# Kernel tuning notes

Measured on AMD Instinct MI355X. Metric: run time of the kernel, lower is better.

The kernel has to match this reference:

```python
import jax, jax.numpy as jnp
import numpy as np
from jax import lax

EPS = 1e-5
HEADS = 8

def chan_ln(x, g):
    # ChanLayerNorm: normalize over channel dim (1), biased variance, gamma only
    mean = jnp.mean(x, axis=1, keepdims=True)
    var = jnp.var(x, axis=1, keepdims=True)
    return (x - mean) * lax.rsqrt(var + EPS) * g[None, :, None, None]

def conv1x1(x, w):  # w: [O, C]
    return jnp.einsum('bchw,oc->bohw', x, w)

def dwconv3(x, w):  # depthwise 3x3, w: [C,1,3,3]
    return lax.conv_general_dilated(x, w, (1, 1), 'SAME',
                                    dimension_numbers=('NCHW', 'OIHW', 'NCHW'),
                                    feature_group_count=x.shape[1])


def setup_inputs() -> dict:
    key = jax.random.key(0)
    ks = jax.random.split(key, 8)
    B, DIM, H, W = 8, 512, 96, 96
    INNER = 256
    s = 0.02
    return {
        'fmap': jax.random.normal(ks[0], (B, DIM, H, W), jnp.float32),
        'norm_g': jnp.ones((DIM,), jnp.float32),
        'q_w1': jax.random.normal(ks[1], (INNER, DIM), jnp.float32) * s,
        'q_wd': jax.random.normal(ks[2], (INNER, 1, 3, 3), jnp.float32) * s,
        'k_w1': jax.random.normal(ks[3], (INNER, DIM), jnp.float32) * s,
        'k_wd': jax.random.normal(ks[4], (INNER, 1, 3, 3), jnp.float32) * s,
        'v_w1': jax.random.normal(ks[5], (INNER, DIM), jnp.float32) * s,
        'v_wd': jax.random.normal(ks[6], (INNER, 1, 3, 3), jnp.float32) * s,
        'out_w': jax.random.normal(ks[7], (DIM, INNER), jnp.float32) * s,
        'out_norm_g': jnp.ones((DIM,), jnp.float32),
    }


def reference(fmap, norm_g, q_w1, q_wd, k_w1, k_wd, v_w1, v_wd, out_w, out_norm_g):
    B, C, H, W = fmap.shape
    inner = q_w1.shape[0]
    dh = inner // HEADS
    scale = dh ** -0.5

    x = chan_ln(fmap, norm_g)
    # dropout is identity in eval mode
    q = dwconv3(conv1x1(x, q_w1), q_wd)
    k = dwconv3(conv1x1(x, k_w1), k_wd)
    v = dwconv3(conv1x1(x, v_w1), v_wd)

    def split(t):  # [B, h*c, H, W] -> [B*h, N, c]
        return t.reshape(B, HEADS, dh, H * W).transpose(0, 1, 3, 2).reshape(B * HEADS, H * W, dh)

    q, k, v = split(q), split(k), split(v)
    q = jax.nn.softmax(q, axis=-1) * scale   # softmax over feature dim
    k = jax.nn.softmax(k, axis=-2)           # softmax over spatial dim

    context = jnp.einsum('bnd,bne->bde', k, v)   # [B*h, d, d]
    out = jnp.einsum('bnd,bde->bne', q, context) # [B*h, N, d]

    out = out.reshape(B, HEADS, H * W, dh).transpose(0, 1, 3, 2).reshape(B, inner, H, W)
    out = jax.nn.silu(out)
    out = conv1x1(out, out_w)
    return chan_ln(out, out_norm_g)
```

## Files before the change

kernel.cpp:

```cpp
#include <hip/hip_runtime.h>
#include <math.h>

#define BATCH 8
#define GB 4
#define CDIM 512
#define HGT 96
#define WID 96
#define HWN (HGT*WID)
#define INNER 256
#define NHEADS 8
#define DH 32
#define NPIX (BATCH*HWN)
#define EPSLN 1e-5f
#define QSCALE 0.17677669529663687f
#define PATHSZ ((size_t)GB*INNER*HWN)

typedef __bf16 bf16_t;
typedef bf16_t bf16x8 __attribute__((ext_vector_type(8)));
typedef float  f32x4  __attribute__((ext_vector_type(4)));

__device__ __forceinline__ void load_lds16(const bf16_t* gp, bf16_t* lp) {
    __builtin_amdgcn_global_load_lds(
        (const __attribute__((address_space(1))) unsigned int*)gp,
        (__attribute__((address_space(3))) unsigned int*)lp,
        16, 0, 0);
}

__global__ __launch_bounds__(256) void wsum_kernel(const float* __restrict__ qw,
                                                   const float* __restrict__ kw,
                                                   const float* __restrict__ vw,
                                                   const float* __restrict__ g,
                                                   float* __restrict__ wsum) {
    int i = blockIdx.x * 256 + threadIdx.x;
    if (i >= 3 * INNER) return;
    const float* w = (i < INNER) ? qw : (i < 2 * INNER) ? kw : vw;
    int o = i % INNER;
    float s = 0.f;
    for (int c = 0; c < CDIM; ++c) s += w[o * CDIM + c] * g[c];
    wsum[i] = s;
}

__global__ __launch_bounds__(256) void wprep_kernel(const float* __restrict__ qw,
                                                    const float* __restrict__ kw,
                                                    const float* __restrict__ vw,
                                                    const float* __restrict__ g,
                                                    const float* __restrict__ ow,
                                                    bf16_t* __restrict__ WB,
                                                    bf16_t* __restrict__ OWB) {
    int i = blockIdx.x * 256 + threadIdx.x;
    const int PS = INNER * CDIM;
    if (i < 3 * PS) {
        int m = i / PS;
        int idx = i % PS;
        int c = idx % CDIM;
        const float* w = (m == 0) ? qw : (m == 1) ? kw : vw;
        float val = w[idx] * g[c];
        bf16_t h = (bf16_t)val;
        bf16_t l = (bf16_t)(val - (float)h);
        WB[(size_t)(2 * m) * PS + idx] = h;
        WB[(size_t)(2 * m + 1) * PS + idx] = l;
    } else {
        int idx = i - 3 * PS;
        float val = ow[idx];
        bf16_t h = (bf16_t)val;
        bf16_t l = (bf16_t)(val - (float)h);
        OWB[idx] = h;
        OWB[PS + idx] = l;
    }
}

__global__ __launch_bounds__(256) void transpose_split_kernel(const float* __restrict__ X,
                                                              bf16_t* __restrict__ Fh,
                                                              bf16_t* __restrict__ Fl,
                                                              float* __restrict__ S1,
                                                              float* __restrict__ S2,
                                                              int pbase) {
    __shared__ float T[64][65];
    __shared__ float Ps[4][64], Ps2[4][64];
    int bb = blockIdx.z;
    int n0 = blockIdx.x * 64;
    int c0 = blockIdx.y * 64;
    const float* Xb = X + ((size_t)bb * CDIM) * HWN;
    int tid = threadIdx.x;
    {
        int nl4 = (tid & 15) * 4;
        int cl = tid >> 4;
        #pragma unroll
        for (int it = 0; it < 4; ++it) {
            int cc = cl + 16 * it;
            f32x4 v = *(const f32x4*)&Xb[(size_t)(c0 + cc) * HWN + n0 + nl4];
            T[cc][nl4]     = v.x;
            T[cc][nl4 + 1] = v.y;
            T[cc][nl4 + 2] = v.z;
            T[cc][nl4 + 3] = v.w;
        }
    }
    int tx = tid & 63, ty = tid >> 6;
    __syncthreads();
    {
        float s = 0.f, s2 = 0.f;
        #pragma unroll
        for (int c = ty * 16; c < ty * 16 + 16; ++c) {
            float v = T[c][tx];
            s += v; s2 += v * v;
        }
        Ps[ty][tx] = s; Ps2[ty][tx] = s2;
    }
    __syncthreads();
    if (tid < 64) {
        float a = Ps[0][tid] + Ps[1][tid] + Ps[2][tid] + Ps[3][tid];
        float b = Ps2[0][tid] + Ps2[1][tid] + Ps2[2][tid] + Ps2[3][tid];
        int p = pbase + bb * HWN + n0 + tid;
        atomicAdd(&S1[p], a);
        atomicAdd(&S2[p], b);
    }
    int nr = tid >> 3;
    int c8 = (tid & 7) << 3;
    size_t obase = ((size_t)bb * HWN) * CDIM;
    #pragma unroll
    for (int half = 0; half < 2; ++half) {
        int n = nr + 32 * half;
        bf16x8 hv, lv;
        #pragma unroll
        for (int j = 0; j < 8; ++j) {
            float v = T[c8 + j][n];
            bf16_t h = (bf16_t)v;
            hv[j] = h;
            lv[j] = (bf16_t)(v - (float)h);
        }
        size_t off = obase + (size_t)(n0 + n) * CDIM + c0 + c8;
        *(bf16x8*)&Fh[off] = hv;
        *(bf16x8*)&Fl[off] = lv;
    }
}

template <int KDIM, int MROWS, int MODE>
__global__ __launch_bounds__(256) void mfma_gemm_kernel(const bf16_t* __restrict__ Wbase,
                                                        const bf16_t* __restrict__ Bh,
                                                        const bf16_t* __restrict__ Bl,
                                                        float* __restrict__ S1,
                                                        float* __restrict__ S2,
                                                        const float* __restrict__ wsum,
                                                        int pbase,
                                                        float* __restrict__ Ybase) {
    __shared__ bf16_t sA[2][128 * 32];
    __shared__ bf16_t sB[2][128 * 32];
    int bb = blockIdx.z;
    int n0 = blockIdx.x * 128;
    const int PS = INNER * CDIM;
    int o0, path;
    const bf16_t *Ah, *Al;
    float* Y;
    if (MODE == 0) {
        path = blockIdx.y >> 1;
        o0 = (blockIdx.y & 1) * 128;
        Ah = Wbase + (size_t)(2 * path) * PS;
        Al = Wbase + (size_t)(2 * path + 1) * PS;
        Y = Ybase + (size_t)path * PATHSZ;
        wsum += path * INNER;
    } else {
        path = 0;
        o0 = blockIdx.y * 128;
        Ah = Wbase;
        Al = Wbase + PS;
        Y = Ybase;
    }
    int tid = threadIdx.x;
    int wv = tid >> 6, ln = tid & 63;
    int wm = wv >> 1, wn = wv & 1;
    int quad = ln >> 4, lm = ln & 15;
    int srow = ln >> 2;
    int scol = ((ln & 3) ^ ((ln >> 3) & 3)) * 8;
    int qs = (quad ^ ((lm >> 1) & 3)) * 8;

    const bf16_t* Bhb = Bh + ((size_t)bb * HWN) * KDIM;
    const bf16_t* Blb = Bl + ((size_t)bb * HWN) * KDIM;

    f32x4 acc[4][4] = {};

    for (int c0 = 0; c0 < KDIM; c0 += 32) {
        __syncthreads();
        #pragma unroll
        for (int t = 0; t < 2; ++t) {
            int inst = wv * 2 + t;
            int row = inst * 16 + srow;
            size_t goA = (size_t)(o0 + row) * KDIM + c0 + scol;
            size_t goB = (size_t)(n0 + row) * KDIM + c0 + scol;
            load_lds16(&Ah[goA],  &sA[0][inst * 512]);
            load_lds16(&Al[goA],  &sA[1][inst * 512]);
            load_lds16(&Bhb[goB], &sB[0][inst * 512]);
            load_lds16(&Blb[goB], &sB[1][inst * 512]);
        }
        __syncthreads();

        bf16x8 afh[4], afl[4], bfh[4], bfl[4];
        #pragma unroll
        for (int i = 0; i < 4; ++i) {
            int o_l = wm * 64 + i * 16 + lm;
            afh[i] = *(const bf16x8*)&sA[0][o_l * 32 + qs];
            afl[i] = *(const bf16x8*)&sA[1][o_l * 32 + qs];
            int n_l = wn * 64 + i * 16 + lm;
            bfh[i] = *(const bf16x8*)&sB[0][n_l * 32 + qs];
            bfl[i] = *(const bf16x8*)&sB[1][n_l * 32 + qs];
        }
        #pragma unroll
        for (int i = 0; i < 4; ++i)
            #pragma unroll
            for (int j = 0; j < 4; ++j) {
                acc[i][j] = __builtin_amdgcn_mfma_f32_16x16x32_bf16(afh[i], bfh[j], acc[i][j], 0, 0, 0);
                acc[i][j] = __builtin_amdgcn_mfma_f32_16x16x32_bf16(afh[i], bfl[j], acc[i][j], 0, 0, 0);
                acc[i][j] = __builtin_amdgcn_mfma_f32_16x16x32_bf16(afl[i], bfh[j], acc[i][j], 0, 0, 0);
            }
    }

    float* Yb = Y + ((size_t)bb * MROWS) * HWN;
    __shared__ float Sn[128], Sn2[128];
    if (MODE == 1) {
        if (tid < 128) Sn[tid] = 0.f; else Sn2[tid - 128] = 0.f;
        __syncthreads();
    }
    #pragma unroll
    for (int j = 0; j < 4; ++j) {
        int nl = wn * 64 + j * 16 + lm;
        int n = n0 + nl;
        float mn = 0.f, rs = 0.f;
        if (MODE == 0) {
            int p = pbase + bb * HWN + n;
            float s1 = S1[p], s2 = S2[p];
            mn = s1 * (1.0f / CDIM);
            float var = s2 * (1.0f / CDIM) - mn * mn;
            rs = rsqrtf(var + EPSLN);
        }
        float js = 0.f, js2 = 0.f;
        #pragma unroll
        for (int i = 0; i < 4; ++i) {
            #pragma unroll
            for (int r = 0; r < 4; ++r) {
                int o = o0 + wm * 64 + i * 16 + quad * 4 + r;
                float v = acc[i][j][r];
                if (MODE == 0) v = rs * (v - mn * wsum[o]);
                Yb[(size_t)o * HWN + n] = v;
                if (MODE == 1) { js += v; js2 += v * v; }
            }
        }
        if (MODE == 1) {
            atomicAdd(&Sn[nl], js);
            atomicAdd(&Sn2[nl], js2);
        }
    }
    if (MODE == 1) {
        __syncthreads();
        if (tid < 128) {
            int p = pbase + bb * HWN + n0 + tid;
            atomicAdd(&S1[p], Sn[tid]);
            atomicAdd(&S2[p], Sn2[tid]);
        }
    }
}

__global__ __launch_bounds__(192) void dwconv_kernel(const float* __restrict__ A3,
                                                     const float* __restrict__ qwd,
                                                     const float* __restrict__ kwd,
                                                     const float* __restrict__ vwd,
                                                     float* __restrict__ D3,
                                                     float* __restrict__ Ssum,
                                                     int bo) {
    int c = blockIdx.y;
    int zz = blockIdx.z;
    int path = zz >> 2;
    int bb = zz & 3;
    const float* wf = ((path == 0) ? qwd : (path == 1) ? kwd : vwd) + c * 9;
    float w[9];
    #pragma unroll
    for (int j = 0; j < 9; ++j) w[j] = wf[j];

    int x0 = threadIdx.x * 4;
    int y0 = (blockIdx.x * 8 + threadIdx.y) * 2;
    bool hasL = (x0 != 0);
    bool hasR = (x0 != WID - 4);

    const float* bp = A3 + (size_t)path * PATHSZ + (size_t)(bb * INNER + c) * HWN;
    f32x4 r[4];
    float L[4], R[4];
    #pragma unroll
    for (int dy = 0; dy < 4; ++dy) {
        int yy = y0 + dy - 1;
        if ((unsigned)yy < HGT) {
            const float* rp = bp + yy * WID + x0;
            r[dy] = *(const f32x4*)rp;
            L[dy] = hasL ? rp[-1] : 0.f;
            R[dy] = hasR ? rp[4]  : 0.f;
        } else {
            r[dy] = (f32x4){0.f, 0.f, 0.f, 0.f};
            L[dy] = 0.f; R[dy] = 0.f;
        }
    }

    f32x4 o[2];
    #pragma unroll
    for (int orow = 0; orow < 2; ++orow) {
        float a0 = 0.f, a1 = 0.f, a2 = 0.f, a3 = 0.f;
        #pragma unroll
        for (int dy = 0; dy < 3; ++dy) {
            f32x4 cv = r[orow + dy];
            float lf = L[orow + dy], rg = R[orow + dy];
            float w0 = w[3 * dy], w1 = w[3 * dy + 1], w2 = w[3 * dy + 2];
            a0 += lf   * w0 + cv.x * w1 + cv.y * w2;
            a1 += cv.x * w0 + cv.y * w1 + cv.z * w2;
            a2 += cv.y * w0 + cv.z * w1 + cv.w * w2;
            a3 += cv.z * w0 + cv.w * w1 + rg   * w2;
        }
        o[orow] = (f32x4){a0, a1, a2, a3};
    }

    size_t ob = (size_t)path * PATHSZ + (size_t)(bb * INNER + c) * HWN;
    if (path == 1) {
        float s = 0.f;
        #pragma unroll
        for (int orow = 0; orow < 2; ++orow) {
            #pragma unroll
            for (int j = 0; j < 4; ++j) {
                float e = __expf(o[orow][j]);
                o[orow][j] = e;
                s += e;
            }
            *(f32x4*)&D3[ob + (size_t)(y0 + orow) * WID + x0] = o[orow];
        }
        #pragma unroll
        for (int off2 = 32; off2; off2 >>= 1) s += __shfl_down(s, off2);
        __shared__ float red[3];
        int tid = threadIdx.y * 24 + threadIdx.x;
        int lane = tid & 63, wvi = tid >> 6;
        if (lane == 0) red[wvi] = s;
        __syncthreads();
        if (tid == 0)
            atomicAdd(&Ssum[(bo + bb) * INNER + c], red[0] + red[1] + red[2]);
    } else {
        *(f32x4*)&D3[ob + (size_t)y0 * WID + x0] = o[0];
        *(f32x4*)&D3[ob + (size_t)(y0 + 1) * WID + x0] = o[1];
    }
}

__global__ __launch_bounds__(256) void context_kernel(const float* __restrict__ K,
                                                      const float* __restrict__ V,
                                                      float* __restrict__ ctxp) {
    int seg = blockIdx.x;
    int bh = blockIdx.y;
    int bb = bh / NHEADS, h = bh % NHEADS;
    const float* kb = K + ((size_t)bb * INNER + h * DH) * HWN;
    const float* vb = V + ((size_t)bb * INNER + h * DH) * HWN;
    __shared__ float kt[DH][64];
    __shared__ float vt[DH][65];
    int tid = threadIdx.x;
    int e = tid & 31;
    int d0 = tid >> 5;
    float acc[4] = {0.f, 0.f, 0.f, 0.f};
    for (int ch = 0; ch < 9; ++ch) {
        int n0 = seg * 576 + ch * 64;
        __syncthreads();
        #pragma unroll
        for (int j = 0; j < 8; ++j) {
            int idx = tid + 256 * j;
            int d = idx >> 6, nn = idx & 63;
            kt[d][nn] = kb[(size_t)d * HWN + n0 + nn];
            vt[d][nn] = vb[(size_t)d * HWN + n0 + nn];
        }
        __syncthreads();
        for (int nn = 0; nn < 64; ++nn) {
            float vv = vt[e][nn];
            #pragma unroll
            for (int i = 0; i < 4; ++i) acc[i] += kt[d0 + 8 * i][nn] * vv;
        }
    }
    #pragma unroll
    for (int i = 0; i < 4; ++i)
        ctxp[(((size_t)bh * 16 + seg) * DH + d0 + 8 * i) * DH + e] = acc[i];
}

__global__ __launch_bounds__(256) void ctxreduce_kernel(const float* __restrict__ ctxp,
                                                        const float* __restrict__ Ssum,
                                                        int bo,
                                                        float* __restrict__ ctx) {
    int i = blockIdx.x * 256 + threadIdx.x;
    int bh = i >> 10, de = i & 1023;
    int d = de >> 5;
    int bb = bh / NHEADS, h = bh % NHEADS;
    float s = 0.f;
    #pragma unroll
    for (int seg = 0; seg < 16; ++seg) s += ctxp[((size_t)bh * 16 + seg) * 1024 + de];
    float S = Ssum[(bo + bb) * INNER + h * DH + d];
    ctx[i] = s / S;
}

__global__ __launch_bounds__(256) void qctx_kernel(const float* __restrict__ Q,
                                                   const float* __restrict__ ctx,
                                                   bf16_t* __restrict__ Oh,
                                                   bf16_t* __restrict__ Ol) {
    int bh = blockIdx.y;
    int bb = bh / NHEADS, h = bh % NHEADS;
    int n = blockIdx.x * 256 + threadIdx.x;
    __shared__ float cs[DH * DH];
    for (int j = threadIdx.x; j < DH * DH; j += 256) cs[j] = ctx[(size_t)bh * DH * DH + j];
    __syncthreads();
    const float* qb = Q + ((size_t)bb * INNER + h * DH) * HWN + n;
    float qv[DH];
    float mx = -1e30f;
    #pragma unroll
    for (int d = 0; d < DH; ++d) { qv[d] = qb[(size_t)d * HWN]; mx = fmaxf(mx, qv[d]); }
    float s = 0.f;
    #pragma unroll
    for (int d = 0; d < DH; ++d) { qv[d] = __expf(qv[d] - mx); s += qv[d]; }
    float inv = QSCALE / s;
    float acc[DH];
    #pragma unroll
    for (int e = 0; e < DH; ++e) acc[e] = 0.f;
    #pragma unroll
    for (int d = 0; d < DH; ++d) {
        float q = qv[d] * inv;
        #pragma unroll
        for (int e = 0; e < DH; ++e) acc[e] += q * cs[d * DH + e];
    }
    size_t ob = ((size_t)bb * HWN + n) * INNER + h * DH;
    bf16x8 hv, lv;
    #pragma unroll
    for (int e8 = 0; e8 < 4; ++e8) {
        #pragma unroll
        for (int e = 0; e < 8; ++e) {
            float x = acc[e8 * 8 + e];
            float sl = x / (1.0f + __expf(-x));
            bf16_t h = (bf16_t)sl;
            hv[e] = h;
            lv[e] = (bf16_t)(sl - (float)h);
        }
        *(bf16x8*)&Oh[ob + e8 * 8] = hv;
        *(bf16x8*)&Ol[ob + e8 * 8] = lv;
    }
}

__global__ __launch_bounds__(256) void norm_kernel(const float* __restrict__ X,
                                                   const float* __restrict__ S1,
                                                   const float* __restrict__ S2,
                                                   const float* __restrict__ g,
                                                   float* __restrict__ out,
                                                   int pbase) {
    size_t i = ((size_t)blockIdx.x * 256 + threadIdx.x) * 4;
    int n = (int)(i % HWN);
    size_t bc = i / HWN;
    int c = (int)(bc % CDIM);
    int bb = (int)(bc / CDIM);
    int p = pbase + bb * HWN + n;
    f32x4 x  = *(const f32x4*)&X[i];
    f32x4 s1 = *(const f32x4*)&S1[p];
    f32x4 s2 = *(const f32x4*)&S2[p];
    float gc = g[c];
    f32x4 o;
    #pragma unroll
    for (int j = 0; j < 4; ++j) {
        float m = s1[j] * (1.0f / CDIM);
        float var = s2[j] * (1.0f / CDIM) - m * m;
        float rs = rsqrtf(var + EPSLN);
        o[j] = (x[j] - m) * rs * gc;
    }
    *(f32x4*)&out[i] = o;
}

extern "C" void kernel_launch(void* const* d_in, const int* in_sizes, int n_in,
                              void* d_out, int out_size, void* d_ws, size_t ws_size,
                              hipStream_t stream) {
    const float* fmap       = (const float*)d_in[0];
    const float* norm_g     = (const float*)d_in[1];
    const float* q_w1       = (const float*)d_in[2];
    const float* q_wd       = (const float*)d_in[3];
    const float* k_w1       = (const float*)d_in[4];
    const float* k_wd       = (const float*)d_in[5];
    const float* v_w1       = (const float*)d_in[6];
    const float* v_wd       = (const float*)d_in[7];
    const float* out_w      = (const float*)d_in[8];
    const float* out_norm_g = (const float*)d_in[9];
    float* out = (float*)d_out;

    float* ws = (float*)d_ws;
    size_t off = 0;
    auto alloc = [&](size_t n) { float* p = ws + off; off += n; return p; };
    float* S1   = alloc(73728);
    float* S2   = alloc(73728);
    float* S1o  = alloc(73728);
    float* S2o  = alloc(73728);
    float* Ssum = alloc(2048);
    const size_t ZERON = 73728ull * 4 + 2048;
    float* wsum = alloc(768);
    bf16_t* WB  = (bf16_t*)alloc(393216);
    bf16_t* OWB = (bf16_t*)alloc(131072);
    float* ctxp = alloc(524288);
    float* ctx  = alloc(32768);
    bf16_t* Fh  = (bf16_t*)alloc(9437184);
    bf16_t* Fl  = (bf16_t*)alloc(9437184);
    float* A3   = alloc(3 * 9437184);
    float* D3   = alloc(3 * 9437184);
    bf16_t* Oh  = (bf16_t*)alloc(4718592);
    bf16_t* Ol  = (bf16_t*)alloc(4718592);
    float* CONV2 = alloc(18874368);

    dim3 blk(256);
    hipMemsetAsync(S1, 0, ZERON * sizeof(float), stream);
    wsum_kernel<<<dim3(3), blk, 0, stream>>>(q_w1, k_w1, v_w1, norm_g, wsum);
    wprep_kernel<<<dim3(2048), blk, 0, stream>>>(q_w1, k_w1, v_w1, norm_g, out_w, WB, OWB);

    for (int g = 0; g < 2; ++g) {
        const float* fmg = fmap + (size_t)g * GB * CDIM * HWN;
        int pbase = g * GB * HWN;
        int bo = g * GB;

        transpose_split_kernel<<<dim3(144, 8, GB), blk, 0, stream>>>(fmg, Fh, Fl, S1, S2, pbase);

        mfma_gemm_kernel<CDIM, INNER, 0><<<dim3(72, 6, GB), blk, 0, stream>>>(
            WB, Fh, Fl, S1, S2, wsum, pbase, A3);

        dwconv_kernel<<<dim3(HGT / 16, INNER, 3 * GB), dim3(24, 8), 0, stream>>>(
            A3, q_wd, k_wd, v_wd, D3, Ssum, bo);

        context_kernel<<<dim3(16, GB * NHEADS), blk, 0, stream>>>(
            D3 + PATHSZ, D3 + 2 * PATHSZ, ctxp);
        ctxreduce_kernel<<<dim3(GB * NHEADS * 1024 / 256), blk, 0, stream>>>(
            ctxp, Ssum, bo, ctx);
        qctx_kernel<<<dim3(HWN / 256, GB * NHEADS), blk, 0, stream>>>(D3, ctx, Oh, Ol);

        mfma_gemm_kernel<INNER, CDIM, 1><<<dim3(72, 4, GB), blk, 0, stream>>>(
            OWB, Oh, Ol, S1o, S2o, nullptr, pbase, CONV2);

        norm_kernel<<<dim3(GB * CDIM * HWN / 1024), blk, 0, stream>>>(
            CONV2, S1o, S2o, out_norm_g, out + (size_t)g * GB * CDIM * HWN, pbase);
    }
}
```

Before: 878.9 us.

## Double-buffer LDS tiles in MFMA GEMM with prefetch two stages ahead

Converts the GEMM K-loop from a single LDS buffer with two barriers per tile into a two-stage ring. Global-to-LDS loads for tile t+2 are issued after the fragments for tile t are read into registers, with explicit vmcnt waits and barriers. MFMA priority is raised during compute. This is meant to hide global load latency behind matrix math, at the cost of doubling LDS use (64KB), which may lower occupancy.

After: 845.3 us, median of 2. 3.8% less time.

```diff
diff --git a/kernel.cpp b/kernel.cpp
--- a/kernel.cpp
+++ b/kernel.cpp
@@ -143,8 +143,8 @@
                                                         const float* __restrict__ wsum,
                                                         int pbase,
                                                         float* __restrict__ Ybase) {
-    __shared__ bf16_t sA[2][128 * 32];
-    __shared__ bf16_t sB[2][128 * 32];
+    __shared__ bf16_t sA[2][2][128 * 32];
+    __shared__ bf16_t sB[2][2][128 * 32];
     int bb = blockIdx.z;
     int n0 = blockIdx.x * 128;
     const int PS = INNER * CDIM;
@@ -178,31 +178,53 @@
 
     f32x4 acc[4][4] = {};
 
-    for (int c0 = 0; c0 < KDIM; c0 += 32) {
-        __syncthreads();
-        #pragma unroll
-        for (int t = 0; t < 2; ++t) {
-            int inst = wv * 2 + t;
+    const int NT = KDIM / 32;
+
+    auto STAGE = [&](int buf, int t) {
+        int c0 = t * 32;
+        #pragma unroll
+        for (int tt = 0; tt < 2; ++tt) {
+            int inst = wv * 2 + tt;
             int row = inst * 16 + srow;
             size_t goA = (size_t)(o0 + row) * KDIM + c0 + scol;
             size_t goB = (size_t)(n0 + row) * KDIM + c0 + scol;
-            load_lds16(&Ah[goA],  &sA[0][inst * 512]);
-            load_lds16(&Al[goA],  &sA[1][inst * 512]);
-            load_lds16(&Bhb[goB], &sB[0][inst * 512]);
-            load_lds16(&Blb[goB], &sB[1][inst * 512]);
-        }
-        __syncthreads();
+            load_lds16(&Ah[goA],  &sA[buf][0][inst * 512]);
+            load_lds16(&Al[goA],  &sA[buf][1][inst * 512]);
+            load_lds16(&Bhb[goB], &sB[buf][0][inst * 512]);
+            load_lds16(&Blb[goB], &sB[buf][1][inst * 512]);
+        }
+    };
+
+    STAGE(0, 0);
+    STAGE(1, 1);
+
+    #pragma unroll 2
+    for (int t = 0; t < NT; ++t) {
+        int buf = t & 1;
+        if (t < NT - 1) asm volatile("s_waitcnt vmcnt(8)" ::: "memory");
+        else            asm volatile("s_waitcnt vmcnt(0)" ::: "memory");
+        __builtin_amdgcn_sched_barrier(0);
+        __builtin_amdgcn_s_barrier();
+        __builtin_amdgcn_sched_barrier(0);
 
         bf16x8 afh[4], afl[4], bfh[4], bfl[4];
         #pragma unroll
         for (int i = 0; i < 4; ++i) {
             int o_l = wm * 64 + i * 16 + lm;
-            afh[i] = *(const bf16x8*)&sA[0][o_l * 32 + qs];
-            afl[i] = *(const bf16x8*)&sA[1][o_l * 32 + qs];
+            afh[i] = *(const bf16x8*)&sA[buf][0][o_l * 32 + qs];
+            afl[i] = *(const bf16x8*)&sA[buf][1][o_l * 32 + qs];
             int n_l = wn * 64 + i * 16 + lm;
-            bfh[i] = *(const bf16x8*)&sB[0][n_l * 32 + qs];
-            bfl[i] = *(const bf16x8*)&sB[1][n_l * 32 + qs];
-        }
+            bfh[i] = *(const bf16x8*)&sB[buf][0][n_l * 32 + qs];
+            bfl[i] = *(const bf16x8*)&sB[buf][1][n_l * 32 + qs];
+        }
+        asm volatile("s_waitcnt lgkmcnt(0)" ::: "memory");
+        __builtin_amdgcn_sched_barrier(0);
+        __builtin_amdgcn_s_barrier();
+        __builtin_amdgcn_sched_barrier(0);
+
+        if (t + 2 < NT) STAGE(buf, t + 2);
+
+        __builtin_amdgcn_s_setprio(1);
         #pragma unroll
         for (int i = 0; i < 4; ++i)
             #pragma unroll
@@ -211,6 +233,7 @@
                 acc[i][j] = __builtin_amdgcn_mfma_f32_16x16x32_bf16(afh[i], bfl[j], acc[i][j], 0, 0, 0);
                 acc[i][j] = __builtin_amdgcn_mfma_f32_16x16x32_bf16(afl[i], bfh[j], acc[i][j], 0, 0, 0);
             }
+        __builtin_amdgcn_s_setprio(0);
     }
 
     float* Yb = Y + ((size_t)bb * MROWS) * HWN;
```
